# Performance work log

Hardware: AMD Instinct MI355X
Metric: run time of the kernel (lower is better)

## Reference

```python
import jax, jax.numpy as jnp
import numpy as np

N = 100000      # nodes
E = 1600000     # edges (avg degree 16)
IN, H, OUT = 128, 64, 32
EPS = 1e-5


def setup_inputs() -> dict:
    key = jax.random.key(0)
    ks = jax.random.split(key, 12)
    g = lambda k, shape, sc: (jax.random.normal(k, shape, jnp.float32) * sc)
    return {
        "x": g(ks[0], (N, IN), 1.0),
        "edge_index": jax.random.randint(ks[1], (2, E), 0, N, dtype=jnp.int32),
        "W1": g(ks[2], (IN, H), (1.0 / IN) ** 0.5), "b1": jnp.zeros((H,), jnp.float32),
        "g1": jnp.ones((H,), jnp.float32), "be1": jnp.zeros((H,), jnp.float32),
        "W2": g(ks[3], (H, H), (1.0 / H) ** 0.5), "b2": jnp.zeros((H,), jnp.float32),
        "g2": jnp.ones((H,), jnp.float32), "be2": jnp.zeros((H,), jnp.float32),
        "Wmu": g(ks[4], (H, OUT), (1.0 / H) ** 0.5), "bmu": jnp.zeros((OUT,), jnp.float32),
        "Wlv": g(ks[5], (H, OUT), (1.0 / H) ** 0.5), "blv": jnp.zeros((OUT,), jnp.float32),
    }


def _gcn_norm(edge_index):
    # add self-loops, compute symmetric deg^-1/2 normalization (PyG GCNConv)
    loop = jnp.arange(N, dtype=edge_index.dtype)
    src = jnp.concatenate([edge_index[0], loop])
    dst = jnp.concatenate([edge_index[1], loop])
    deg = jax.ops.segment_sum(jnp.ones_like(src, jnp.float32), dst, num_segments=N)
    dinv = jnp.where(deg > 0, jax.lax.rsqrt(jnp.maximum(deg, 1.0)), 0.0)
    norm = dinv[src] * dinv[dst]  # [E+N]
    return src, dst, norm


def _gcn_conv(h, W, b, src, dst, norm):
    h = h @ W                              # [N, out] dense transform first
    msg = h[src] * norm[:, None]           # gather + scale  [E+N, out]
    agg = jax.ops.segment_sum(msg, dst, num_segments=N)  # scatter-add
    return agg + b


def _batchnorm(h, gamma, beta):
    mu = h.mean(axis=0)
    var = h.var(axis=0)
    return (h - mu) * jax.lax.rsqrt(var + EPS) * gamma + beta


def reference(x, edge_index, W1, b1, g1, be1, W2, b2, g2, be2, Wmu, bmu, Wlv, blv):
    src, dst, norm = _gcn_norm(edge_index)
    h = jax.nn.relu(_batchnorm(_gcn_conv(x, W1, b1, src, dst, norm), g1, be1))
    h = jax.nn.relu(_batchnorm(_gcn_conv(h, W2, b2, src, dst, norm), g2, be2))
    mu = _gcn_conv(h, Wmu, bmu, src, dst, norm)
    logvar = _gcn_conv(h, Wlv, blv, src, dst, norm)
    return (mu, logvar)
```

## Files before the change

kernel.cpp:

```cpp
#include <hip/hip_runtime.h>

#define NNODES 100000
#define NEDGES 1600000
#define KBUCK 196
#define RNG 512
#define BCAP 9216
#define CHUNK 4096
#define NBAGG 2048
#define NRED 128

typedef __attribute__((ext_vector_type(8))) short bf16x8_t;
typedef __attribute__((ext_vector_type(4))) float f32x4_t;

__device__ inline unsigned short f2bf(float f) {
    union { float f; unsigned u; } a; a.f = f;
    unsigned r = (a.u + 0x7FFFu + ((a.u >> 16) & 1u)) >> 16;
    return (unsigned short)r;
}

__device__ inline void addpk(float acc[4], uint2 v) {
    union { unsigned u; float f; } t0, t1, t2, t3;
    t0.u = v.x << 16;          acc[0] += t0.f;
    t1.u = v.x & 0xFFFF0000u;  acc[1] += t1.f;
    t2.u = v.y << 16;          acc[2] += t2.f;
    t3.u = v.y & 0xFFFF0000u;  acc[3] += t3.f;
}

__global__ __launch_bounds__(256) void k_bin(
    const int* __restrict__ src, const int* __restrict__ dst,
    unsigned int* __restrict__ gbuf, int* __restrict__ gcount, int e)
{
    __shared__ unsigned int bins[KBUCK][64];
    __shared__ int bcount[KBUCK];
    const int tid = threadIdx.x;
    for (int i = tid; i < KBUCK; i += 256) bcount[i] = 0;
    __syncthreads();

    int base = blockIdx.x * CHUNK;
    int lim = min(e, base + CHUNK);
    for (int i = base + tid; i < lim; i += 256) {
        int d = dst[i];
        int s = src[i];
        int b = d >> 9;
        unsigned int entry = ((unsigned int)(d & 511) << 17) | (unsigned int)s;
        int idx = atomicAdd(&bcount[b], 1);
        if (idx < 64) {
            bins[b][idx] = entry;
        } else {
            int gpos = atomicAdd(&gcount[b], 1);
            if (gpos < BCAP) gbuf[(size_t)b * BCAP + gpos] = entry;
        }
    }
    __syncthreads();

    for (int b = tid; b < KBUCK; b += 256) {
        int n = min(bcount[b], 64);
        if (n > 0) {
            int pos = atomicAdd(&gcount[b], n);
            int m = min(n, BCAP - pos);
            for (int i = 0; i < m; ++i)
                gbuf[(size_t)b * BCAP + pos + i] = bins[b][i];
        }
    }
}

__global__ __launch_bounds__(256) void k_hist_dinv(
    const unsigned int* __restrict__ gbuf, const int* __restrict__ gcount,
    int* __restrict__ deg, float* __restrict__ dinv, int n)
{
    __shared__ int hist[RNG];
    const int b = blockIdx.x, tid = threadIdx.x;
    for (int i = tid; i < RNG; i += 256) hist[i] = 0;
    __syncthreads();
    int cnt = gcount[b];
    const unsigned int* buf = gbuf + (size_t)b * BCAP;
    for (int j = tid; j < cnt; j += 256)
        atomicAdd(&hist[buf[j] >> 17], 1);
    __syncthreads();
    int nbase = b * RNG;
    for (int i = tid; i < RNG; i += 256) {
        int node = nbase + i;
        if (node < n) {
            int dgi = hist[i];
            deg[node] = dgi;
            dinv[node] = rsqrtf((float)(dgi + 1));
        }
    }
}

__global__ __launch_bounds__(256) void k_block_reduce(const int* __restrict__ deg,
                                                      int* __restrict__ partials, int n) {
    __shared__ int red[256];
    int b = blockIdx.x, t = threadIdx.x;
    int base = b * 1024;
    int v = 0;
    for (int i = t; i < 1024; i += 256) {
        int idx = base + i;
        if (idx < n) v += deg[idx];
    }
    red[t] = v; __syncthreads();
    for (int s = 128; s > 0; s >>= 1) { if (t < s) red[t] += red[t + s]; __syncthreads(); }
    if (t == 0) partials[b] = red[0];
}

__global__ void k_scan_partials(int* partials, int nb) {
    if (threadIdx.x == 0 && blockIdx.x == 0) {
        int run = 0;
        for (int i = 0; i < nb; ++i) { int v = partials[i]; partials[i] = run; run += v; }
    }
}

__global__ __launch_bounds__(256) void k_block_scan(const int* __restrict__ deg,
                                                    const int* __restrict__ partials,
                                                    int* __restrict__ rowptr, int n, int etot) {
    __shared__ int red[256];
    int b = blockIdx.x, t = threadIdx.x;
    int base = b * 1024 + t * 4;
    int d[4]; int s = 0;
    for (int j = 0; j < 4; ++j) {
        int idx = base + j;
        d[j] = (idx < n) ? deg[idx] : 0;
        s += d[j];
    }
    red[t] = s; __syncthreads();
    for (int off = 1; off < 256; off <<= 1) {
        int v = (t >= off) ? red[t - off] : 0;
        __syncthreads();
        red[t] += v;
        __syncthreads();
    }
    int excl = partials[b] + (t > 0 ? red[t - 1] : 0);
    for (int j = 0; j < 4; ++j) {
        int idx = base + j;
        if (idx < n) rowptr[idx] = excl;
        excl += d[j];
    }
    if (b == 0 && t == 0) rowptr[n] = etot;
}

__global__ __launch_bounds__(256) void k_fill_local(
    const unsigned int* __restrict__ gbuf, const int* __restrict__ gcount,
    const int* __restrict__ rowptr, int* __restrict__ adj, int n)
{
    __shared__ int cursor[RNG];
    const int b = blockIdx.x, tid = threadIdx.x;
    int nbase = b * RNG;
    for (int i = tid; i < RNG; i += 256) {
        int node = nbase + i;
        cursor[i] = (node < n) ? rowptr[node] : 0;
    }
    __syncthreads();
    int cnt = gcount[b];
    const unsigned int* buf = gbuf + (size_t)b * BCAP;
    for (int j = tid; j < cnt; j += 256) {
        unsigned int e = buf[j];
        int dl = e >> 17;
        int s = (int)(e & 0x1FFFFu);
        int pos = atomicAdd(&cursor[dl], 1);
        adj[pos] = s;
    }
}

__global__ void k_prep_w(const float* __restrict__ W1, const float* __restrict__ W2,
                         const float* __restrict__ Wmu, const float* __restrict__ Wlv,
                         unsigned short* __restrict__ Wt1, unsigned short* __restrict__ Wt2,
                         unsigned short* __restrict__ Wtc) {
    int i = blockIdx.x * 256 + threadIdx.x;
    if (i < 64 * 128) {
        int nn = i >> 7, kk = i & 127;
        Wt1[i] = f2bf(W1[kk * 64 + nn]);
    }
    if (i < 64 * 64) {
        int nn = i >> 6, kk = i & 63;
        Wt2[i] = f2bf(W2[kk * 64 + nn]);
        Wtc[i] = f2bf(nn < 32 ? Wmu[kk * 32 + nn] : Wlv[kk * 32 + (nn - 32)]);
    }
}

template <int K, bool TRANS>
__global__ __launch_bounds__(256) void k_gemm_mfma(
    const float* __restrict__ A, const unsigned short* __restrict__ Wt,
    const float* __restrict__ dinv, const float* __restrict__ alpha,
    const float* __restrict__ delta, unsigned short* __restrict__ U, int n)
{
    constexpr int SK = K + 8;
    __shared__ unsigned short As[64 * SK];
    __shared__ unsigned short Ws[64 * SK];
    const int tid = threadIdx.x;
    const int brow = blockIdx.x * 64;
    const int lane = tid & 63, wv = tid >> 6;

    for (int i = tid; i < 64 * (K / 4); i += 256) {
        int r = i / (K / 4), c4 = i % (K / 4);
        *reinterpret_cast<ushort4*>(&Ws[r * SK + c4 * 4]) =
            reinterpret_cast<const ushort4*>(Wt)[i];
    }
    for (int i = tid; i < 64 * (K / 4); i += 256) {
        int r = i / (K / 4), c4 = i % (K / 4);
        int grow = brow + r;
        ushort4 o = {0, 0, 0, 0};
        if (grow < n) {
            float4 v = reinterpret_cast<const float4*>(A)[(size_t)grow * (K / 4) + c4];
            if (TRANS) {
                float dv = dinv[grow];
                int c = c4 * 4;
                v.x = fmaxf(fmaf(v.x * dv, alpha[c + 0], delta[c + 0]), 0.f);
                v.y = fmaxf(fmaf(v.y * dv, alpha[c + 1], delta[c + 1]), 0.f);
                v.z = fmaxf(fmaf(v.z * dv, alpha[c + 2], delta[c + 2]), 0.f);
                v.w = fmaxf(fmaf(v.w * dv, alpha[c + 3], delta[c + 3]), 0.f);
            }
            o.x = f2bf(v.x); o.y = f2bf(v.y); o.z = f2bf(v.z); o.w = f2bf(v.w);
        }
        *reinterpret_cast<ushort4*>(&As[r * SK + c4 * 4]) = o;
    }
    __syncthreads();

    f32x4_t acc[4] = {{0.f, 0.f, 0.f, 0.f}, {0.f, 0.f, 0.f, 0.f},
                      {0.f, 0.f, 0.f, 0.f}, {0.f, 0.f, 0.f, 0.f}};
    const int ar = (wv << 4) + (lane & 15);
    const int kq = (lane >> 4) * 8;
#pragma unroll
    for (int kc = 0; kc < K / 32; ++kc) {
        bf16x8_t a = *reinterpret_cast<const bf16x8_t*>(&As[ar * SK + kc * 32 + kq]);
#pragma unroll
        for (int c = 0; c < 4; ++c) {
            bf16x8_t b = *reinterpret_cast<const bf16x8_t*>(
                &Ws[(c * 16 + (lane & 15)) * SK + kc * 32 + kq]);
            acc[c] = __builtin_amdgcn_mfma_f32_16x16x32_bf16(a, b, acc[c], 0, 0, 0);
        }
    }

    unsigned short* Cs = As;
#pragma unroll
    for (int r = 0; r < 4; ++r) {
        int lrow = (wv << 4) + ((lane >> 4) << 2) + r;
        int grow = brow + lrow;
        float dv = (grow < n) ? dinv[grow] : 0.f;
#pragma unroll
        for (int c = 0; c < 4; ++c)
            Cs[lrow * 72 + c * 16 + (lane & 15)] = f2bf(acc[c][r] * dv);
    }
    __syncthreads();
    for (int i = tid; i < 64 * 8; i += 256) {
        int r = i >> 3, g = i & 7;
        int grow = brow + r;
        if (grow < n)
            *reinterpret_cast<uint4*>(&U[(size_t)grow * 64 + g * 8]) =
                *reinterpret_cast<const uint4*>(&Cs[r * 72 + g * 8]);
    }
}

__device__ inline void gather_row4(const int* __restrict__ rowptr, const int* __restrict__ adj,
                                   const uint2* __restrict__ u2, int node, int lane, int q, int f16,
                                   float acc[4])
{
    int beg = rowptr[node], end = rowptr[node + 1];
    for (int cbeg = beg; cbeg < end; cbeg += 64) {
        int cnt = min(64, end - cbeg);
        int a = (lane < cnt) ? adj[cbeg + lane] : 0;
        int T = (cnt + 3) >> 2;
        int t = 0, i = q;
        for (; t + 4 <= T; t += 4, i += 16) {
            int s0 = __shfl(a, i);
            int s1 = __shfl(a, i + 4);
            int s2 = __shfl(a, i + 8);
            int s3 = __shfl(a, i + 12);
            uint2 v0 = u2[(size_t)s0 * 16 + f16];
            uint2 v1 = u2[(size_t)s1 * 16 + f16];
            uint2 v2 = u2[(size_t)s2 * 16 + f16];
            uint2 v3 = u2[(size_t)s3 * 16 + f16];
            if (i      >= cnt) { v0.x = 0u; v0.y = 0u; }
            if (i + 4  >= cnt) { v1.x = 0u; v1.y = 0u; }
            if (i + 8  >= cnt) { v2.x = 0u; v2.y = 0u; }
            if (i + 12 >= cnt) { v3.x = 0u; v3.y = 0u; }
            addpk(acc, v0); addpk(acc, v1); addpk(acc, v2); addpk(acc, v3);
        }
        for (; t < T; ++t, i += 4) {
            int s = __shfl(a, i);
            uint2 v = u2[(size_t)s * 16 + f16];
            if (i >= cnt) { v.x = 0u; v.y = 0u; }
            addpk(acc, v);
        }
    }
}

template <int MODE>
__global__ __launch_bounds__(256) void k_agg4(
    const int* __restrict__ rowptr, const int* __restrict__ adj,
    const uint2* __restrict__ u2, const float* __restrict__ dinv,
    const float* __restrict__ bias,
    const float* __restrict__ bmu, const float* __restrict__ blv,
    float* __restrict__ sout, float* __restrict__ outp,
    float* __restrict__ pblk, int n)
{
    const int tid = threadIdx.x;
    const int lane = tid & 63;
    const int q = lane >> 4, f16 = lane & 15;
    const int wv = tid >> 6;
    const int wid = (blockIdx.x * 256 + tid) >> 6;
    const int nw = (gridDim.x * 256) >> 6;

    float4 bb;
    if (MODE == 0) {
        bb = *reinterpret_cast<const float4*>(&bias[f16 * 4]);
    } else {
        bb = (f16 < 8) ? *reinterpret_cast<const float4*>(&bmu[f16 * 4])
                       : *reinterpret_cast<const float4*>(&blv[(f16 - 8) * 4]);
    }

    float ls[4] = {0.f, 0.f, 0.f, 0.f}, lq[4] = {0.f, 0.f, 0.f, 0.f};

    for (int node = wid; node < n; node += nw) {
        float acc[4] = {0.f, 0.f, 0.f, 0.f};
        gather_row4(rowptr, adj, u2, node, lane, q, f16, acc);
        if (q == 0) {
            uint2 vs = u2[(size_t)node * 16 + f16];
            addpk(acc, vs);
        }
#pragma unroll
        for (int j = 0; j < 4; ++j) {
            acc[j] += __shfl_xor(acc[j], 16);
            acc[j] += __shfl_xor(acc[j], 32);
        }
        if (q == 0) {
            if (MODE == 0) {
                float4 o = {acc[0], acc[1], acc[2], acc[3]};
                *reinterpret_cast<float4*>(&sout[(size_t)node * 64 + f16 * 4]) = o;
                float dv = dinv[node];
                float y0 = fmaf(acc[0], dv, bb.x); ls[0] += y0; lq[0] = fmaf(y0, y0, lq[0]);
                float y1 = fmaf(acc[1], dv, bb.y); ls[1] += y1; lq[1] = fmaf(y1, y1, lq[1]);
                float y2 = fmaf(acc[2], dv, bb.z); ls[2] += y2; lq[2] = fmaf(y2, y2, lq[2]);
                float y3 = fmaf(acc[3], dv, bb.w); ls[3] += y3; lq[3] = fmaf(y3, y3, lq[3]);
            } else {
                float dv = dinv[node];
                float4 o = {fmaf(acc[0], dv, bb.x), fmaf(acc[1], dv, bb.y),
                            fmaf(acc[2], dv, bb.z), fmaf(acc[3], dv, bb.w)};
                size_t total = (size_t)n * 32;
                float* dst = (f16 < 8) ? &outp[(size_t)node * 32 + f16 * 4]
                                       : &outp[total + (size_t)node * 32 + (f16 - 8) * 4];
                *reinterpret_cast<float4*>(dst) = o;
            }
        }
    }

    if (MODE == 0) {
        __shared__ float red[4][128];
        if (q == 0) {
#pragma unroll
            for (int j = 0; j < 4; ++j) {
                red[wv][f16 * 4 + j] = ls[j];
                red[wv][64 + f16 * 4 + j] = lq[j];
            }
        }
        __syncthreads();
        if (tid < 128) {
            float v = red[0][tid] + red[1][tid] + red[2][tid] + red[3][tid];
            pblk[(size_t)blockIdx.x * 128 + tid] = v;
        }
    }
}

__global__ __launch_bounds__(256) void k_reduce_pblk(
    const float* __restrict__ pblk, float* __restrict__ pblk2, int nb)
{
    __shared__ float red[2][128];
    int b = blockIdx.x, t = threadIdx.x;
    int col = t & 127, rg = t >> 7;
    int rows = nb / NRED;
    int base = b * rows;
    float s = 0.f;
    for (int r = rg; r < rows; r += 2) s += pblk[(size_t)(base + r) * 128 + col];
    red[rg][col] = s;
    __syncthreads();
    if (t < 128) pblk2[(size_t)b * 128 + t] = red[0][t] + red[1][t];
}

__global__ __launch_bounds__(256) void k_bn_finalize2(
    const float* __restrict__ pblk, int nb,
    const float* __restrict__ g, const float* __restrict__ be,
    const float* __restrict__ b, float* __restrict__ alpha,
    float* __restrict__ delta, int n)
{
    __shared__ float tmp[256];
    __shared__ float stats[128];
    int t = threadIdx.x;
    int col = t & 127, half = t >> 7;
    float s = 0.f;
    for (int b2 = half; b2 < nb; b2 += 2) s += pblk[(size_t)b2 * 128 + col];
    tmp[t] = s; __syncthreads();
    if (t < 128) stats[t] = tmp[t] + tmp[t + 128];
    __syncthreads();
    if (t < 64) {
        float mu = stats[t] / (float)n;
        float var = stats[64 + t] / (float)n - mu * mu;
        float inv = rsqrtf(var + 1e-5f);
        float a = inv * g[t];
        alpha[t] = a;
        delta[t] = fmaf(b[t] - mu, a, be[t]);
    }
}

extern "C" void kernel_launch(void* const* d_in, const int* in_sizes, int n_in,
                              void* d_out, int out_size, void* d_ws, size_t ws_size,
                              hipStream_t stream) {
    const int N = NNODES, E = NEDGES;

    const float* x   = (const float*)d_in[0];
    const int* ei    = (const int*)d_in[1];
    const float* W1  = (const float*)d_in[2];
    const float* b1  = (const float*)d_in[3];
    const float* g1  = (const float*)d_in[4];
    const float* be1 = (const float*)d_in[5];
    const float* W2  = (const float*)d_in[6];
    const float* b2  = (const float*)d_in[7];
    const float* g2  = (const float*)d_in[8];
    const float* be2 = (const float*)d_in[9];
    const float* Wmu = (const float*)d_in[10];
    const float* bmu = (const float*)d_in[11];
    const float* Wlv = (const float*)d_in[12];
    const float* blv = (const float*)d_in[13];
    float* out = (float*)d_out;

    const int* src = ei;
    const int* dst = ei + E;

    char* ws = (char*)d_ws;
    size_t off = 0;
    auto alloc = [&](size_t bytes) { char* p = ws + off; off += (bytes + 255) & ~(size_t)255; return p; };
    float*          dinv   = (float*)alloc((size_t)N * 4);
    unsigned short* bufU   = (unsigned short*)alloc((size_t)N * 64 * 2);
    float*          bufS   = (float*)alloc((size_t)N * 64 * 4);
    int*            degi   = (int*)alloc((size_t)N * 4);
    int*            rowptr = (int*)alloc((size_t)(N + 1) * 4);
    int*            adj    = (int*)alloc((size_t)E * 4);
    unsigned int*   gbuf   = (unsigned int*)alloc((size_t)KBUCK * BCAP * 4);
    int*            gcount = (int*)alloc((size_t)KBUCK * 4);
    int*            partials = (int*)alloc(128 * 4);
    float*          pblk   = (float*)alloc((size_t)NBAGG * 128 * 4);
    float*          pblk2  = (float*)alloc((size_t)NRED * 128 * 4);
    unsigned short* Wt1    = (unsigned short*)alloc(64 * 128 * 2);
    unsigned short* Wt2    = (unsigned short*)alloc(64 * 64 * 2);
    unsigned short* Wtc    = (unsigned short*)alloc(64 * 64 * 2);
    float*          alpha  = (float*)alloc(64 * 4);
    float*          delta  = (float*)alloc(64 * 4);
    (void)ws_size;

    const int B = 256;
    dim3 blk(B);
    int gGemm  = (N + 63) / 64;
    int gScan  = (N + 1023) / 1024;
    int gBin   = (E + CHUNK - 1) / CHUNK;
    const uint2* u2 = (const uint2*)bufU;

    hipMemsetAsync(gcount, 0, (size_t)KBUCK * 4, stream);
    k_bin<<<gBin, blk, 0, stream>>>(src, dst, gbuf, gcount, E);
    k_hist_dinv<<<KBUCK, blk, 0, stream>>>(gbuf, gcount, degi, dinv, N);
    k_block_reduce<<<gScan, blk, 0, stream>>>(degi, partials, N);
    k_scan_partials<<<1, 64, 0, stream>>>(partials, gScan);
    k_block_scan<<<gScan, blk, 0, stream>>>(degi, partials, rowptr, N, E);
    k_fill_local<<<KBUCK, blk, 0, stream>>>(gbuf, gcount, rowptr, adj, N);
    k_prep_w<<<32, blk, 0, stream>>>(W1, W2, Wmu, Wlv, Wt1, Wt2, Wtc);

    k_gemm_mfma<128, false><<<gGemm, blk, 0, stream>>>(x, Wt1, dinv, nullptr, nullptr, bufU, N);
    k_agg4<0><<<NBAGG, blk, 0, stream>>>(rowptr, adj, u2, dinv, b1, nullptr, nullptr,
                                         bufS, nullptr, pblk, N);
    k_reduce_pblk<<<NRED, blk, 0, stream>>>(pblk, pblk2, NBAGG);
    k_bn_finalize2<<<1, blk, 0, stream>>>(pblk2, NRED, g1, be1, b1, alpha, delta, N);

    k_gemm_mfma<64, true><<<gGemm, blk, 0, stream>>>(bufS, Wt2, dinv, alpha, delta, bufU, N);
    k_agg4<0><<<NBAGG, blk, 0, stream>>>(rowptr, adj, u2, dinv, b2, nullptr, nullptr,
                                         bufS, nullptr, pblk, N);
    k_reduce_pblk<<<NRED, blk, 0, stream>>>(pblk, pblk2, NBAGG);
    k_bn_finalize2<<<1, blk, 0, stream>>>(pblk2, NRED, g2, be2, b2, alpha, delta, N);

    k_gemm_mfma<64, true><<<gGemm, blk, 0, stream>>>(bufS, Wtc, dinv, alpha, delta, bufU, N);
    k_agg4<1><<<NBAGG, blk, 0, stream>>>(rowptr, adj, u2, dinv, nullptr, bmu, blv,
                                         nullptr, out, nullptr, N);
}
```

Before: 264.5 us.

## Store intermediate aggregation buffer in bf16 and use packed float2 accumulation

The pre-batchnorm aggregation output bufS becomes bf16 instead of fp32, halving its write in the aggregation kernel and its read in the next GEMM's transform step. The gather accumulation also moves to two-wide float vectors so the compiler can emit packed adds. The cost is extra rounding of the hidden activations before batchnorm, which may affect accuracy. Batch statistics are still computed from the fp32 accumulators.

```diff
diff --git a/kernel.cpp b/kernel.cpp
--- a/kernel.cpp
+++ b/kernel.cpp
@@ -11,19 +11,25 @@
 
 typedef __attribute__((ext_vector_type(8))) short bf16x8_t;
 typedef __attribute__((ext_vector_type(4))) float f32x4_t;
+typedef __attribute__((ext_vector_type(2))) float f32x2_t;
 
 __device__ inline unsigned short f2bf(float f) {
     union { float f; unsigned u; } a; a.f = f;
     unsigned r = (a.u + 0x7FFFu + ((a.u >> 16) & 1u)) >> 16;
     return (unsigned short)r;
 }
-
-__device__ inline void addpk(float acc[4], uint2 v) {
-    union { unsigned u; float f; } t0, t1, t2, t3;
-    t0.u = v.x << 16;          acc[0] += t0.f;
-    t1.u = v.x & 0xFFFF0000u;  acc[1] += t1.f;
-    t2.u = v.y << 16;          acc[2] += t2.f;
-    t3.u = v.y & 0xFFFF0000u;  acc[3] += t3.f;
+__device__ inline float bfbits_lo(unsigned u) {
+    union { unsigned u; float f; } a; a.u = u << 16; return a.f;
+}
+__device__ inline float bfbits_hi(unsigned u) {
+    union { unsigned u; float f; } a; a.u = u & 0xFFFF0000u; return a.f;
+}
+
+__device__ inline void addpk2(f32x2_t& a01, f32x2_t& a23, uint2 v) {
+    f32x2_t d0, d1;
+    d0.x = bfbits_lo(v.x); d0.y = bfbits_hi(v.x);
+    d1.x = bfbits_lo(v.y); d1.y = bfbits_hi(v.y);
+    a01 += d0; a23 += d1;
 }
 
 __global__ __launch_bounds__(256) void k_bin(
@@ -179,7 +185,7 @@
 
 template <int K, bool TRANS>
 __global__ __launch_bounds__(256) void k_gemm_mfma(
-    const float* __restrict__ A, const unsigned short* __restrict__ Wt,
+    const void* __restrict__ Av, const unsigned short* __restrict__ Wt,
     const float* __restrict__ dinv, const float* __restrict__ alpha,
     const float* __restrict__ delta, unsigned short* __restrict__ U, int n)
 {
@@ -200,16 +206,21 @@
         int grow = brow + r;
         ushort4 o = {0, 0, 0, 0};
         if (grow < n) {
-            float4 v = reinterpret_cast<const float4*>(A)[(size_t)grow * (K / 4) + c4];
             if (TRANS) {
+                uint2 sv = reinterpret_cast<const uint2*>(Av)[(size_t)grow * (K / 4) + c4];
+                float f0 = bfbits_lo(sv.x), f1 = bfbits_hi(sv.x);
+                float f2 = bfbits_lo(sv.y), f3 = bfbits_hi(sv.y);
                 float dv = dinv[grow];
                 int c = c4 * 4;
-                v.x = fmaxf(fmaf(v.x * dv, alpha[c + 0], delta[c + 0]), 0.f);
-                v.y = fmaxf(fmaf(v.y * dv, alpha[c + 1], delta[c + 1]), 0.f);
-                v.z = fmaxf(fmaf(v.z * dv, alpha[c + 2], delta[c + 2]), 0.f);
-                v.w = fmaxf(fmaf(v.w * dv, alpha[c + 3], delta[c + 3]), 0.f);
+                f0 = fmaxf(fmaf(f0 * dv, alpha[c + 0], delta[c + 0]), 0.f);
+                f1 = fmaxf(fmaf(f1 * dv, alpha[c + 1], delta[c + 1]), 0.f);
+                f2 = fmaxf(fmaf(f2 * dv, alpha[c + 2], delta[c + 2]), 0.f);
+                f3 = fmaxf(fmaf(f3 * dv, alpha[c + 3], delta[c + 3]), 0.f);
+                o.x = f2bf(f0); o.y = f2bf(f1); o.z = f2bf(f2); o.w = f2bf(f3);
+            } else {
+                float4 v = reinterpret_cast<const float4*>(Av)[(size_t)grow * (K / 4) + c4];
+                o.x = f2bf(v.x); o.y = f2bf(v.y); o.z = f2bf(v.z); o.w = f2bf(v.w);
             }
-            o.x = f2bf(v.x); o.y = f2bf(v.y); o.z = f2bf(v.z); o.w = f2bf(v.w);
         }
         *reinterpret_cast<ushort4*>(&As[r * SK + c4 * 4]) = o;
     }
@@ -252,7 +263,7 @@
 
 __device__ inline void gather_row4(const int* __restrict__ rowptr, const int* __restrict__ adj,
                                    const uint2* __restrict__ u2, int node, int lane, int q, int f16,
-                                   float acc[4])
+                                   f32x2_t& a01, f32x2_t& a23)
 {
     int beg = rowptr[node], end = rowptr[node + 1];
     for (int cbeg = beg; cbeg < end; cbeg += 64) {
@@ -273,13 +284,14 @@
             if (i + 4  >= cnt) { v1.x = 0u; v1.y = 0u; }
             if (i + 8  >= cnt) { v2.x = 0u; v2.y = 0u; }
             if (i + 12 >= cnt) { v3.x = 0u; v3.y = 0u; }
-            addpk(acc, v0); addpk(acc, v1); addpk(acc, v2); addpk(acc, v3);
+            addpk2(a01, a23, v0); addpk2(a01, a23, v1);
+            addpk2(a01, a23, v2); addpk2(a01, a23, v3);
         }
         for (; t < T; ++t, i += 4) {
             int s = __shfl(a, i);
             uint2 v = u2[(size_t)s * 16 + f16];
             if (i >= cnt) { v.x = 0u; v.y = 0u; }
-            addpk(acc, v);
+            addpk2(a01, a23, v);
         }
     }
 }
@@ -290,7 +302,7 @@
     const uint2* __restrict__ u2, const float* __restrict__ dinv,
     const float* __restrict__ bias,
     const float* __restrict__ bmu, const float* __restrict__ blv,
-    float* __restrict__ sout, float* __restrict__ outp,
+    unsigned short* __restrict__ sout, float* __restrict__ outp,
     float* __restrict__ pblk, int n)
 {
     const int tid = threadIdx.x;
@@ -311,30 +323,30 @@
     float ls[4] = {0.f, 0.f, 0.f, 0.f}, lq[4] = {0.f, 0.f, 0.f, 0.f};
 
     for (int node = wid; node < n; node += nw) {
-        float acc[4] = {0.f, 0.f, 0.f, 0.f};
-        gather_row4(rowptr, adj, u2, node, lane, q, f16, acc);
+        f32x2_t a01 = {0.f, 0.f}, a23 = {0.f, 0.f};
+        gather_row4(rowptr, adj, u2, node, lane, q, f16, a01, a23);
         if (q == 0) {
-            uint2 vs = u2[(size_t)node * 16 + f16];
-            addpk(acc, vs);
-        }
-#pragma unroll
-        for (int j = 0; j < 4; ++j) {
-            acc[j] += __shfl_xor(acc[j], 16);
-            acc[j] += __shfl_xor(acc[j], 32);
-        }
+            addpk2(a01, a23, u2[(size_t)node * 16 + f16]);
+        }
+        a01.x += __shfl_xor(a01.x, 16); a01.x += __shfl_xor(a01.x, 32);
+        a01.y += __shfl_xor(a01.y, 16); a01.y += __shfl_xor(a01.y, 32);
+        a23.x += __shfl_xor(a23.x, 16); a23.x += __shfl_xor(a23.x, 32);
+        a23.y += __shfl_xor(a23.y, 16); a23.y += __shfl_xor(a23.y, 32);
         if (q == 0) {
             if (MODE == 0) {
-                float4 o = {acc[0], acc[1], acc[2], acc[3]};
-                *reinterpret_cast<float4*>(&sout[(size_t)node * 64 + f16 * 4]) = o;
+                uint2 o;
+                o.x = (unsigned)f2bf(a01.x) | ((unsigned)f2bf(a01.y) << 16);
+                o.y = (unsigned)f2bf(a23.x) | ((unsigned)f2bf(a23.y) << 16);
+                reinterpret_cast<uint2*>(sout)[(size_t)node * 16 + f16] = o;
                 float dv = dinv[node];
-                float y0 = fmaf(acc[0], dv, bb.x); ls[0] += y0; lq[0] = fmaf(y0, y0, lq[0]);
-                float y1 = fmaf(acc[1], dv, bb.y); ls[1] += y1; lq[1] = fmaf(y1, y1, lq[1]);
-                float y2 = fmaf(acc[2], dv, bb.z); ls[2] += y2; lq[2] = fmaf(y2, y2, lq[2]);
-                float y3 = fmaf(acc[3], dv, bb.w); ls[3] += y3; lq[3] = fmaf(y3, y3, lq[3]);
+                float y0 = fmaf(a01.x, dv, bb.x); ls[0] += y0; lq[0] = fmaf(y0, y0, lq[0]);
+                float y1 = fmaf(a01.y, dv, bb.y); ls[1] += y1; lq[1] = fmaf(y1, y1, lq[1]);
+                float y2 = fmaf(a23.x, dv, bb.z); ls[2] += y2; lq[2] = fmaf(y2, y2, lq[2]);
+                float y3 = fmaf(a23.y, dv, bb.w); ls[3] += y3; lq[3] = fmaf(y3, y3, lq[3]);
             } else {
                 float dv = dinv[node];
-                float4 o = {fmaf(acc[0], dv, bb.x), fmaf(acc[1], dv, bb.y),
-                            fmaf(acc[2], dv, bb.z), fmaf(acc[3], dv, bb.w)};
+                float4 o = {fmaf(a01.x, dv, bb.x), fmaf(a01.y, dv, bb.y),
+                            fmaf(a23.x, dv, bb.z), fmaf(a23.y, dv, bb.w)};
                 size_t total = (size_t)n * 32;
                 float* dst = (f16 < 8) ? &outp[(size_t)node * 32 + f16 * 4]
                                        : &outp[total + (size_t)node * 32 + (f16 - 8) * 4];
@@ -429,7 +441,7 @@
     auto alloc = [&](size_t bytes) { char* p = ws + off; off += (bytes + 255) & ~(size_t)255; return p; };
     float*          dinv   = (float*)alloc((size_t)N * 4);
     unsigned short* bufU   = (unsigned short*)alloc((size_t)N * 64 * 2);
-    float*          bufS   = (float*)alloc((size_t)N * 64 * 4);
+    unsigned short* bufS   = (unsigned short*)alloc((size_t)N * 64 * 2);
     int*            degi   = (int*)alloc((size_t)N * 4);
     int*            rowptr = (int*)alloc((size_t)(N + 1) * 4);
     int*            adj    = (int*)alloc((size_t)E * 4);
```

Result: no change. 269.6 us (+1.9%).
